# Optimization experiments

Hardware: AMD Instinct MI355X
Metric: run time of the kernel (lower is better)

## Reference

```python
import jax, jax.numpy as jnp
import numpy as np

EPS = 1e-5
NUM_HEADS = 16
HEAD_DIM = 64


def layernorm(x, g, b):
    mu = jnp.mean(x, axis=-1, keepdims=True)
    var = jnp.mean(jnp.square(x - mu), axis=-1, keepdims=True)
    return (x - mu) * jax.lax.rsqrt(var + EPS) * g + b


def setup_inputs() -> dict:
    key = jax.random.key(0)
    ks = jax.random.split(key, 10)
    B, S, Q, D = 4, 4096, 256, 1024
    x = jax.random.normal(ks[0], (B, S, D), dtype=jnp.float32)
    queries = jax.random.normal(ks[1], (B, Q, D), dtype=jnp.float32)
    attn_mask = jax.random.randint(ks[2], (B, NUM_HEADS, Q, S), 0, 2) == 1
    key_padding_mask = jax.random.randint(ks[3], (B, S), 0, 2) == 1
    scale = 1.0 / np.sqrt(2.0 * D)  # xavier-ish
    Wq = jax.random.normal(ks[4], (D, D), dtype=jnp.float32) * scale
    Wk = jax.random.normal(ks[5], (D, D), dtype=jnp.float32) * scale
    Wv = jax.random.normal(ks[6], (D, D), dtype=jnp.float32) * scale
    Wo = jax.random.normal(ks[7], (D, D), dtype=jnp.float32) * scale
    ln1_g = jnp.ones((D,), jnp.float32); ln1_b = jnp.zeros((D,), jnp.float32)
    ln2_g = jnp.ones((D,), jnp.float32); ln2_b = jnp.zeros((D,), jnp.float32)
    return {"x": x, "queries": queries, "attn_mask": attn_mask,
            "key_padding_mask": key_padding_mask, "Wq": Wq, "Wk": Wk,
            "Wv": Wv, "Wo": Wo, "ln1_g": ln1_g, "ln1_b": ln1_b,
            "ln2_g": ln2_g, "ln2_b": ln2_b}


def reference(x, queries, attn_mask, key_padding_mask, Wq, Wk, Wv, Wo,
              ln1_g, ln1_b, ln2_g, ln2_b):
    B, S, D = x.shape
    Q = queries.shape[1]
    H, hd = NUM_HEADS, HEAD_DIM

    xn = layernorm(x, ln1_g, ln1_b)
    q = (queries @ Wq.T).reshape(B, Q, H, hd)
    k = (xn @ Wk.T).reshape(B, S, H, hd)
    v = (xn @ Wv.T).reshape(B, S, H, hd)

    # scores: (B, H, Q, S)
    scores = jnp.einsum('bqhd,bshd->bhqs', q, k) / np.sqrt(hd)

    mask = attn_mask | key_padding_mask[:, None, None, :]
    neg_inf = jnp.float32(-jnp.inf)
    masked = jnp.where(mask, neg_inf, scores)
    all_masked = jnp.all(mask, axis=-1, keepdims=True)  # rows fully masked
    safe = jnp.where(all_masked, 0.0, masked)
    attn = jax.nn.softmax(safe, axis=-1)
    attn = jnp.where(all_masked, 0.0, attn)

    out = jnp.einsum('bhqs,bshd->bqhd', attn, v).reshape(B, Q, D)
    out = layernorm(out, ln2_g, ln2_b)
    return out @ Wo.T, attn.mean(axis=1)
```

## Files before the change

### kernel.cpp

```cpp
#include <hip/hip_runtime.h>
#include <math.h>

#define DEV __device__ __forceinline__

typedef float  f4v  __attribute__((ext_vector_type(4)));
typedef __bf16 b8v  __attribute__((ext_vector_type(8)));
typedef short  s8v  __attribute__((ext_vector_type(8)));

DEV short f2b(float f){ __bf16 h = (__bf16)f; return __builtin_bit_cast(short, h); }
DEV float b2f(short s){ __bf16 h = __builtin_bit_cast(__bf16, s); return (float)h; }

DEV void gload16(const void* g, void* l){
  __builtin_amdgcn_global_load_lds((const __attribute__((address_space(1))) void*)g,
                                   (__attribute__((address_space(3))) void*)l, 16, 0, 0);
}

DEV b8v ldsf(const short* p){ return __builtin_bit_cast(b8v, *(const s8v*)p); }

DEV f4v mfma16(b8v a, b8v b, f4v c){ return __builtin_amdgcn_mfma_f32_16x16x32_bf16(a, b, c, 0, 0, 0); }

DEV void lds_barrier(){
  asm volatile("s_waitcnt lgkmcnt(0)" ::: "memory");
  __builtin_amdgcn_s_barrier();
}

__global__ __launch_bounds__(256) void prep_kernel(const float* __restrict__ x, const float* __restrict__ ln1g,
                                                   const float* __restrict__ ln1b, short* __restrict__ xn,
                                                   const float* __restrict__ s0, const float* __restrict__ s1,
                                                   const float* __restrict__ s2, const float* __restrict__ s3,
                                                   const float* __restrict__ s4,
                                                   short* __restrict__ d0, short* __restrict__ d1,
                                                   short* __restrict__ d2, short* __restrict__ d3,
                                                   short* __restrict__ d4){
  int bid = blockIdx.x, tid = threadIdx.x;
  if (bid < 5120){
    int i = bid*256 + tid;
    int buf = i >> 18, j = i & 262143;
    const float* s = (buf==0)?s0:(buf==1)?s1:(buf==2)?s2:(buf==3)?s3:s4;
    short*       d = (buf==0)?d0:(buf==1)?d1:(buf==2)?d2:(buf==3)?d3:d4;
    float4 v = ((const float4*)s)[j];
    ((short4*)d)[j] = make_short4(f2b(v.x), f2b(v.y), f2b(v.z), f2b(v.w));
    return;
  }
  int row = bid - 5120;
  const float4 v = ((const float4*)(x + (size_t)row*1024))[tid];
  float s = v.x + v.y + v.z + v.w;
  #pragma unroll
  for (int off=1; off<64; off<<=1) s += __shfl_xor(s, off);
  __shared__ float red[4];
  if ((tid&63)==0) red[tid>>6] = s;
  __syncthreads();
  float mu = (red[0]+red[1]+red[2]+red[3]) * (1.0f/1024.0f);
  float e0=v.x-mu, e1=v.y-mu, e2=v.z-mu, e3=v.w-mu;
  float q = e0*e0 + e1*e1 + e2*e2 + e3*e3;
  #pragma unroll
  for (int off=1; off<64; off<<=1) q += __shfl_xor(q, off);
  __syncthreads();
  if ((tid&63)==0) red[tid>>6] = q;
  __syncthreads();
  float rs = rsqrtf((red[0]+red[1]+red[2]+red[3]) * (1.0f/1024.0f) + 1e-5f);
  float4 g4 = ((const float4*)ln1g)[tid];
  float4 b4 = ((const float4*)ln1b)[tid];
  short4 o = make_short4(f2b(e0*rs*g4.x + b4.x), f2b(e1*rs*g4.y + b4.y),
                         f2b(e2*rs*g4.z + b4.z), f2b(e3*rs*g4.w + b4.w));
  ((short4*)(xn + (size_t)row*1024))[tid] = o;
}

__global__ __launch_bounds__(256) void ln_reduce_kernel(const short* __restrict__ opart, const float* __restrict__ gg,
                                                        const float* __restrict__ bb, short* __restrict__ out){
  int row = blockIdx.x, tid = threadIdx.x;
  float a0=0.f, a1=0.f, a2=0.f, a3=0.f;
  #pragma unroll
  for (int sc=0; sc<32; ++sc){
    short4 t = ((const short4*)(opart + ((size_t)sc*1024 + row)*1024))[tid];
    a0 += b2f(t.x); a1 += b2f(t.y); a2 += b2f(t.z); a3 += b2f(t.w);
  }
  float s = a0 + a1 + a2 + a3;
  #pragma unroll
  for (int off=1; off<64; off<<=1) s += __shfl_xor(s, off);
  __shared__ float red[4];
  if ((tid&63)==0) red[tid>>6] = s;
  __syncthreads();
  float mu = (red[0]+red[1]+red[2]+red[3]) * (1.0f/1024.0f);
  float d0=a0-mu, d1=a1-mu, d2=a2-mu, d3=a3-mu;
  float q = d0*d0 + d1*d1 + d2*d2 + d3*d3;
  #pragma unroll
  for (int off=1; off<64; off<<=1) q += __shfl_xor(q, off);
  __syncthreads();
  if ((tid&63)==0) red[tid>>6] = q;
  __syncthreads();
  float rs = rsqrtf((red[0]+red[1]+red[2]+red[3]) * (1.0f/1024.0f) + 1e-5f);
  float4 g4 = ((const float4*)gg)[tid];
  float4 b4 = ((const float4*)bb)[tid];
  short4 o = make_short4(f2b(d0*rs*g4.x + b4.x), f2b(d1*rs*g4.y + b4.y),
                         f2b(d2*rs*g4.z + b4.z), f2b(d3*rs*g4.w + b4.w));
  ((short4*)(out + (size_t)row*1024))[tid] = o;
}

template<int OUTF32>
__global__ __launch_bounds__(256) void gemm_small(const short* __restrict__ A, const short* __restrict__ B,
                                                  void* __restrict__ C, int M, int N, int K){
  __shared__ short sA[2][64*64];
  __shared__ short sB[2][64*64];
  int tid=threadIdx.x, lane=tid&63, wv=tid>>6, g=lane>>4, r=lane&15;
  int wr=wv>>1, wc=wv&1;
  int m0=blockIdx.x*64, n0=blockIdx.y*64;
  f4v z = {0.f,0.f,0.f,0.f};
  f4v acc[2][2];
  #pragma unroll
  for (int i=0;i<2;++i){
    #pragma unroll
    for (int j=0;j<2;++j) acc[i][j]=z;
  }
  auto stage = [&](int buf, int kt){
    #pragma unroll
    for (int i=0;i<2;++i){
      int idx = i*256 + tid;
      int row = idx>>3, cbs = (idx&7)^(row&7);
      gload16(A + (size_t)(m0+row)*K + kt*64 + cbs*8, &sA[buf][(i*256+wv*64)*8]);
      gload16(B + (size_t)(n0+row)*K + kt*64 + cbs*8, &sB[buf][(i*256+wv*64)*8]);
    }
  };
  int nkt = K >> 6;
  stage(0, 0);
  for (int kt=0; kt<nkt; ++kt){
    int cur = kt & 1;
    if (kt+1 < nkt){
      stage(cur^1, kt+1);
      asm volatile("s_waitcnt vmcnt(4)" ::: "memory");
    } else {
      asm volatile("s_waitcnt vmcnt(0)" ::: "memory");
    }
    __builtin_amdgcn_s_barrier();
    b8v af[2][2], bf[2][2];
    #pragma unroll
    for (int mf=0;mf<2;++mf){
      #pragma unroll
      for (int ks=0;ks<2;++ks){
        int ra = wr*32 + mf*16 + r;
        int rb = wc*32 + mf*16 + r;
        af[mf][ks] = ldsf(&sA[cur][ra*64 + (((ks*4+g)^(ra&7))*8)]);
        bf[mf][ks] = ldsf(&sB[cur][rb*64 + (((ks*4+g)^(rb&7))*8)]);
      }
    }
    #pragma unroll
    for (int mf=0;mf<2;++mf){
      #pragma unroll
      for (int nf=0;nf<2;++nf){
        acc[mf][nf] = mfma16(af[mf][0], bf[nf][0], acc[mf][nf]);
        acc[mf][nf] = mfma16(af[mf][1], bf[nf][1], acc[mf][nf]);
      }
    }
    asm volatile("s_waitcnt lgkmcnt(0)" ::: "memory");
    __builtin_amdgcn_s_barrier();
  }
  #pragma unroll
  for (int mf=0;mf<2;++mf){
    #pragma unroll
    for (int nf=0;nf<2;++nf){
      #pragma unroll
      for (int j=0;j<4;++j){
        int m = m0 + wr*32 + mf*16 + g*4 + j;
        int n = n0 + wc*32 + nf*16 + r;
        if (OUTF32) ((float*)C)[(size_t)m*N + n] = acc[mf][nf][j];
        else        ((short*)C)[(size_t)m*N + n] = f2b(acc[mf][nf][j]);
      }
    }
  }
}

__global__ __launch_bounds__(512,2) void gemm_dual_bt(const short* __restrict__ A, const short* __restrict__ B0,
                                                      const short* __restrict__ B1, short* __restrict__ C0,
                                                      short* __restrict__ vt, int M, int N, int K){
  __shared__ short sA[2][256*32];
  __shared__ short sB0[2][128*32];
  __shared__ short sB1[2][128*32];
  int tid=threadIdx.x, lane=tid&63, wv=tid>>6, g=lane>>4, r=lane&15;
  int wr=wv>>1, wc=wv&1;
  int m0=blockIdx.x*256, n0=blockIdx.y*128;
  f4v z = {0.f,0.f,0.f,0.f};
  f4v a0[4][4], a1[4][4];
  #pragma unroll
  for (int i=0;i<4;++i){
    #pragma unroll
    for (int j=0;j<4;++j){ a0[i][j]=z; a1[i][j]=z; }
  }
  auto stage = [&](int buf, int kt){
    #pragma unroll
    for (int i=0;i<2;++i){
      int idx = i*512 + tid;
      int row = idx>>2, sl = (idx&3)^(row&3);
      gload16(A + (size_t)(m0+row)*K + kt*32 + sl*8, &sA[buf][(i*512+wv*64)*8]);
    }
    {
      int row = tid>>2, sl = (tid&3)^(row&3);
      gload16(B0 + (size_t)(n0+row)*K + kt*32 + sl*8, &sB0[buf][(wv*64)*8]);
      gload16(B1 + (size_t)(n0+row)*K + kt*32 + sl*8, &sB1[buf][(wv*64)*8]);
    }
  };
  int nkt = K >> 5;
  stage(0, 0);
  for (int kt=0; kt<nkt; ++kt){
    int cur = kt & 1;
    if (kt+1 < nkt){
      stage(cur^1, kt+1);
      asm volatile("s_waitcnt vmcnt(4)" ::: "memory");
    } else {
      asm volatile("s_waitcnt vmcnt(0)" ::: "memory");
    }
    __builtin_amdgcn_s_barrier();
    b8v af[4], b0f[4], b1f[4];
    #pragma unroll
    for (int mf=0;mf<4;++mf){
      int ra = wr*64+mf*16+r;
      af[mf] = ldsf(&sA[cur][ra*32 + ((g^(ra&3))*8)]);
    }
    #pragma unroll
    for (int nf=0;nf<4;++nf){
      int rb = wc*64+nf*16+r;
      b0f[nf] = ldsf(&sB0[cur][rb*32 + ((g^(rb&3))*8)]);
      b1f[nf] = ldsf(&sB1[cur][rb*32 + ((g^(rb&3))*8)]);
    }
    #pragma unroll
    for (int mf=0;mf<4;++mf){
      #pragma unroll
      for (int nf=0;nf<4;++nf){
        a0[mf][nf] = mfma16(af[mf], b0f[nf], a0[mf][nf]);
        a1[mf][nf] = mfma16(af[mf], b1f[nf], a1[mf][nf]);
      }
    }
    asm volatile("s_waitcnt lgkmcnt(0)" ::: "memory");
    __builtin_amdgcn_s_barrier();
  }
  int b = m0 >> 12;
  #pragma unroll
  for (int mf=0;mf<4;++mf){
    #pragma unroll
    for (int nf=0;nf<4;++nf){
      int m = m0 + wr*64 + mf*16 + g*4;
      int n = n0 + wc*64 + nf*16 + r;
      #pragma unroll
      for (int j=0;j<4;++j)
        C0[(size_t)(m+j)*N + n] = f2b(a0[mf][nf][j]);
      int h = n >> 6, hd = n & 63;
      short4 vv = make_short4(f2b(a1[mf][nf][0]), f2b(a1[mf][nf][1]),
                              f2b(a1[mf][nf][2]), f2b(a1[mf][nf][3]));
      *(short4*)&vt[(size_t)((b*16 + h)*64 + hd)*4096 + (m & 4095)] = vv;
    }
  }
}

__global__ __launch_bounds__(256,2) void lsum_kernel(const short* __restrict__ qp, const short* __restrict__ kb,
                                                     const int* __restrict__ am, const int* __restrict__ kpm,
                                                     unsigned* __restrict__ pm, float* __restrict__ lpart){
  int bid = blockIdx.x;
  int sc = bid & 15, bh = bid >> 4;
  int b = bh >> 4, h = bh & 15;
  int s0 = sc*256;
  __shared__ short sQ[256*64];
  __shared__ short sK[256*64];
  __shared__ unsigned sPM[256*8];
  int tid=threadIdx.x, lane=tid&63, wv=tid>>6, g=lane>>4, r=lane&15;

  #pragma unroll
  for (int i=0;i<8;++i){
    int idx = i*256 + wv*64 + lane;
    int row = idx>>3, cbs = (idx&7)^(row&7);
    gload16(qp + (size_t)(b*256 + row)*1024 + h*64 + cbs*8, &sQ[(i*256+wv*64)*8]);
  }
  #pragma unroll
  for (int i=0;i<8;++i){
    int idx = i*256 + wv*64 + lane;
    int row = idx>>3, cbs = (idx&7)^(row&7);
    gload16(kb + (size_t)(b*4096 + s0 + row)*1024 + h*64 + cbs*8, &sK[(i*256+wv*64)*8]);
  }
  int4 kp = *(const int4*)(kpm + (size_t)b*4096 + s0 + lane*4);
  bool k0 = kp.x!=0, k1 = kp.y!=0, k2 = kp.z!=0, k3 = kp.w!=0;
  #pragma unroll 4
  for (int i=0;i<64;++i){
    int row = wv*64 + i;
    const int4 t = *(const int4*)(am + (size_t)(bh*256 + row)*4096 + s0 + lane*4);
    unsigned long long m0 = __ballot(k0 || (t.x!=0));
    unsigned long long m1 = __ballot(k1 || (t.y!=0));
    unsigned long long m2 = __ballot(k2 || (t.z!=0));
    unsigned long long m3 = __ballot(k3 || (t.w!=0));
    if (lane < 8){
      int jj = lane>>1, hh = lane&1;
      unsigned long long bj = (jj==0)?m0:((jj==1)?m1:((jj==2)?m2:m3));
      unsigned w = (unsigned)(bj >> (hh*32));
      sPM[row*8 + lane] = w;
      pm[(size_t)bid*2048 + row*8 + lane] = w;
    }
  }
  __syncthreads();

  b8v a[4][2];
  #pragma unroll
  for (int mf=0;mf<4;++mf){
    #pragma unroll
    for (int ks=0;ks<2;++ks){
      int q = wv*64 + mf*16 + r;
      a[mf][ks] = ldsf(&sQ[q*64 + (((ks*4+g)^(q&7))*8)]);
    }
  }
  unsigned wmr[4][4][2];
  #pragma unroll
  for (int mf=0;mf<4;++mf){
    #pragma unroll
    for (int jq=0;jq<4;++jq){
      int q = wv*64 + mf*16 + g*4 + jq;
      wmr[mf][jq][0] = sPM[q*8 + (r&3)*2 + 0];
      wmr[mf][jq][1] = sPM[q*8 + (r&3)*2 + 1];
    }
  }
  float lacc[4][4];
  #pragma unroll
  for (int mf=0;mf<4;++mf){
    #pragma unroll
    for (int j=0;j<4;++j) lacc[mf][j] = 0.f;
  }
  f4v z = {0.f,0.f,0.f,0.f};
  #pragma unroll 4
  for (int nf=0;nf<16;++nf){
    int srow = nf*16 + r;
    b8v b0 = ldsf(&sK[srow*64 + ((g^(srow&7))*8)]);
    b8v b1 = ldsf(&sK[srow*64 + (((4+g)^(srow&7))*8)]);
    f4v acc[4];
    #pragma unroll
    for (int mf=0;mf<4;++mf){
      acc[mf] = mfma16(a[mf][0], b0, z);
      acc[mf] = mfma16(a[mf][1], b1, acc[mf]);
    }
    int bitp = 4*(nf&7) + (r>>2);
    #pragma unroll
    for (int mf=0;mf<4;++mf){
      #pragma unroll
      for (int j=0;j<4;++j){
        bool mskd = (wmr[mf][j][nf>>3] >> bitp) & 1u;
        lacc[mf][j] += mskd ? 0.f : __expf(acc[mf][j]*0.125f);
      }
    }
  }
  #pragma unroll
  for (int off=1; off<16; off<<=1){
    #pragma unroll
    for (int mf=0;mf<4;++mf){
      #pragma unroll
      for (int j=0;j<4;++j) lacc[mf][j] += __shfl_xor(lacc[mf][j], off);
    }
  }
  if (r == 0){
    #pragma unroll
    for (int mf=0;mf<4;++mf){
      #pragma unroll
      for (int j=0;j<4;++j){
        int q = wv*64 + mf*16 + g*4 + j;
        lpart[(size_t)bid*256 + q] = lacc[mf][j];
      }
    }
  }
}

__global__ void lcomb_kernel(const float* __restrict__ lpart, float* __restrict__ linv){
  int row = blockIdx.x*256 + threadIdx.x;
  int q = row & 255, bh = row >> 8;
  float l = 0.f;
  #pragma unroll
  for (int sc=0; sc<16; ++sc) l += lpart[(size_t)(bh*16+sc)*256 + q];
  linv[row] = (l > 0.f) ? (1.0f/l) : 0.f;
}

__global__ __launch_bounds__(512,4) void attn_pv_kernel(const short* __restrict__ qp, const short* __restrict__ kb,
                                                        const short* __restrict__ vt, const unsigned* __restrict__ pm,
                                                        const float* __restrict__ linv, short* __restrict__ opart,
                                                        float* __restrict__ out2){
  int bid = blockIdx.x;
  int sc = bid & 31, qt = (bid>>5)&3, b = bid>>7;
  int s0 = sc*128, q0 = qt*64;
  int half = sc & 1, scq = sc >> 1;
  __shared__ short sK[128*64];
  __shared__ short sV[64*128];
  __shared__ short sQ[64*64];
  __shared__ unsigned sPM[64*4];
  int tid=threadIdx.x, lane=tid&63, wv=tid>>6, g=lane>>4, r=lane&15;
  int wq = wv>>2, ws = wv&3;
  f4v z = {0.f,0.f,0.f,0.f};
  float macc[2][2][4];
  #pragma unroll
  for (int sb=0;sb<2;++sb){
    #pragma unroll
    for (int qb=0;qb<2;++qb){
      #pragma unroll
      for (int j=0;j<4;++j) macc[sb][qb][j] = 0.f;
    }
  }

  for (int h=0; h<16; ++h){
    int bh = b*16 + h;
    { int row = tid>>3, cbs = (tid&7)^(row&7);
      gload16(qp + (size_t)(b*256 + q0 + row)*1024 + h*64 + cbs*8, &sQ[(wv*64)*8]); }
    #pragma unroll
    for (int i=0;i<2;++i){
      int idx = i*512 + tid;
      int row = idx>>3, cbs = (idx&7)^(row&7);
      gload16(kb + (size_t)(b*4096 + s0 + row)*1024 + h*64 + cbs*8, &sK[(i*512+wv*64)*8]);
    }
    #pragma unroll
    for (int i=0;i<2;++i){
      int idx = i*512 + tid;
      int row = idx>>4, sl = idx&15, sls = sl^(row&7);
      gload16(vt + (size_t)(bh*64 + row)*4096 + s0 + sls*8, &sV[(i*512+wv*64)*8]);
    }
    if (tid < 256)
      sPM[tid] = pm[(size_t)(bh*16+scq)*2048 + (q0 + (tid>>2))*8 + (tid&3)*2 + half];
    __syncthreads();

    b8v qf[2][2];
    #pragma unroll
    for (int qb=0;qb<2;++qb){
      #pragma unroll
      for (int ks=0;ks<2;++ks){
        int qrow = wq*32 + qb*16 + r;
        qf[qb][ks] = ldsf(&sQ[qrow*64 + (((ks*4+g)^(qrow&7))*8)]);
      }
    }
    f4v accs[2][2];
    __builtin_amdgcn_s_setprio(1);
    #pragma unroll
    for (int sb=0;sb<2;++sb){
      int srow = ws*32 + sb*16 + r;
      b8v k0 = ldsf(&sK[srow*64 + ((g^(srow&7))*8)]);
      b8v k1 = ldsf(&sK[srow*64 + (((4+g)^(srow&7))*8)]);
      #pragma unroll
      for (int qb=0;qb<2;++qb){
        accs[sb][qb] = mfma16(k0, qf[qb][0], z);
        accs[sb][qb] = mfma16(k1, qf[qb][1], accs[sb][qb]);
      }
    }
    __builtin_amdgcn_s_setprio(0);
    lds_barrier();

    float iv[2];
    iv[0] = linv[(size_t)bh*256 + q0 + wq*32 + r];
    iv[1] = linv[(size_t)bh*256 + q0 + wq*32 + 16 + r];
    unsigned wmq[2][4];
    #pragma unroll
    for (int qb=0;qb<2;++qb){
      #pragma unroll
      for (int j=0;j<4;++j)
        wmq[qb][j] = sPM[(wq*32+qb*16+r)*4 + j];
    }
    short* P = &sK[0];
    #pragma unroll
    for (int sb=0;sb<2;++sb){
      int bitp = ws*8 + sb*4 + g;
      #pragma unroll
      for (int qb=0;qb<2;++qb){
        float pj[4];
        #pragma unroll
        for (int j=0;j<4;++j){
          bool mskd = (wmq[qb][j] >> bitp) & 1u;
          pj[j] = mskd ? 0.f : __expf(accs[sb][qb][j]*0.125f) * iv[qb];
          macc[sb][qb][j] += pj[j];
        }
        int q = wq*32 + qb*16 + r;
        unsigned lo = ((unsigned)(unsigned short)f2b(pj[0])) | (((unsigned)(unsigned short)f2b(pj[1]))<<16);
        unsigned hi = ((unsigned)(unsigned short)f2b(pj[2])) | (((unsigned)(unsigned short)f2b(pj[3]))<<16);
        int sbase = (ws*32 + sb*16 + g*4) ^ ((q&7)<<3);
        uint2 pk; pk.x = lo; pk.y = hi;
        *(uint2*)&P[q*128 + sbase] = pk;
      }
    }
    lds_barrier();

    f4v acco[2]; acco[0]=z; acco[1]=z;
    __builtin_amdgcn_s_setprio(1);
    #pragma unroll
    for (int ks=0;ks<4;++ks){
      int vrow = ws*16 + r;
      b8v bv = ldsf(&sV[vrow*128 + ((ks*32+g*8) ^ ((vrow&7)<<3))]);
      #pragma unroll
      for (int mf=0;mf<2;++mf){
        int prow = wq*32 + mf*16 + r;
        b8v ap = ldsf(&P[prow*128 + ((ks*32+g*8) ^ ((prow&7)<<3))]);
        acco[mf] = mfma16(ap, bv, acco[mf]);
      }
    }
    __builtin_amdgcn_s_setprio(0);
    #pragma unroll
    for (int mf=0;mf<2;++mf){
      #pragma unroll
      for (int j=0;j<4;++j)
        opart[((size_t)sc*1024 + b*256 + q0 + wq*32 + mf*16 + g*4 + j)*1024 + h*64 + ws*16 + r] = f2b(acco[mf][j]);
    }
    lds_barrier();
  }

  #pragma unroll
  for (int sb=0;sb<2;++sb){
    #pragma unroll
    for (int qb=0;qb<2;++qb){
      int q = q0 + wq*32 + qb*16 + r;
      float4 o = make_float4(macc[sb][qb][0]*0.0625f, macc[sb][qb][1]*0.0625f,
                             macc[sb][qb][2]*0.0625f, macc[sb][qb][3]*0.0625f);
      *(float4*)&out2[(size_t)(b*256 + q)*4096 + s0 + ws*32 + sb*16 + g*4] = o;
    }
  }
}

extern "C" void kernel_launch(void* const* d_in, const int* in_sizes, int n_in,
                              void* d_out, int out_size, void* d_ws, size_t ws_size,
                              hipStream_t stream){
  const float* x       = (const float*)d_in[0];
  const float* queries = (const float*)d_in[1];
  const int*   am      = (const int*)d_in[2];
  const int*   kpm     = (const int*)d_in[3];
  const float* Wq      = (const float*)d_in[4];
  const float* Wk      = (const float*)d_in[5];
  const float* Wv      = (const float*)d_in[6];
  const float* Wo      = (const float*)d_in[7];
  const float* ln1g    = (const float*)d_in[8];
  const float* ln1b    = (const float*)d_in[9];
  const float* ln2g    = (const float*)d_in[10];
  const float* ln2b    = (const float*)d_in[11];
  float* out0 = (float*)d_out;
  float* out2 = out0 + (size_t)4*256*1024;
  char* ws = (char*)d_ws;

  size_t off = 0;
  auto alloc = [&](size_t bytes){ void* p = ws + off; off += (bytes + 255) & ~(size_t)255; return p; };
  short*    xn   = (short*)alloc(33554432);
  short*    kb   = (short*)alloc(33554432);
  short*    vt   = (short*)alloc(33554432);
  short*    wqb  = (short*)alloc(2097152);
  short*    wkb  = (short*)alloc(2097152);
  short*    wvb  = (short*)alloc(2097152);
  short*    wob  = (short*)alloc(2097152);
  short*    qbf  = (short*)alloc(2097152);
  short*    qpj  = (short*)alloc(2097152);
  unsigned* pmw  = (unsigned*)alloc(8388608);
  float*    lpart= (float*)alloc(1048576);
  float*    linv = (float*)alloc(65536);
  short*    opart= (short*)alloc(67108864);
  short*    onb  = (short*)alloc(2097152);

  prep_kernel<<<21504,256,0,stream>>>(x, ln1g, ln1b, xn,
                                      queries, Wq, Wk, Wv, Wo, qbf, wqb, wkb, wvb, wob);
  gemm_dual_bt<<<dim3(64,8),512,0,stream>>>(xn, wkb, wvb, kb, vt, 16384, 1024, 1024);
  gemm_small<0><<<dim3(16,16),256,0,stream>>>(qbf, wqb, qpj, 1024, 1024, 1024);
  lsum_kernel<<<1024,256,0,stream>>>(qpj, kb, am, kpm, pmw, lpart);
  lcomb_kernel<<<64,256,0,stream>>>(lpart, linv);
  attn_pv_kernel<<<512,512,0,stream>>>(qpj, kb, vt, pmw, linv, opart, out2);
  ln_reduce_kernel<<<1024,256,0,stream>>>(opart, ln2g, ln2b, onb);
  gemm_small<1><<<dim3(16,16),256,0,stream>>>(onb, wob, out0, 1024, 1024, 1024);
}
```

Before: 325.5 us.

## Replace dual K/V GEMM with 256x256-tile 8-wave pipelined GEMM launched twice

New measurement: 323.3 us. About the same (-0.7%).

```diff
diff --git a/kernel.cpp b/kernel.cpp
--- a/kernel.cpp
+++ b/kernel.cpp
@@ -169,83 +169,156 @@
   }
 }
 
-__global__ __launch_bounds__(512,2) void gemm_dual_bt(const short* __restrict__ A, const short* __restrict__ B0,
-                                                      const short* __restrict__ B1, short* __restrict__ C0,
-                                                      short* __restrict__ vt, int M, int N, int K){
-  __shared__ short sA[2][256*32];
-  __shared__ short sB0[2][128*32];
-  __shared__ short sB1[2][128*32];
+template<int VT>
+__global__ __launch_bounds__(512,1) void gemm8_bt(const short* __restrict__ A, const short* __restrict__ B,
+                                                  short* __restrict__ C){
+  __shared__ short sA[2][256*64];
+  __shared__ short sB[2][256*64];
   int tid=threadIdx.x, lane=tid&63, wv=tid>>6, g=lane>>4, r=lane&15;
-  int wr=wv>>1, wc=wv&1;
-  int m0=blockIdx.x*256, n0=blockIdx.y*128;
+  int wr=wv>>2, wc=wv&3;
+  int m0 = blockIdx.x*256, n0 = blockIdx.y*256;
   f4v z = {0.f,0.f,0.f,0.f};
-  f4v a0[4][4], a1[4][4];
-  #pragma unroll
-  for (int i=0;i<4;++i){
-    #pragma unroll
-    for (int j=0;j<4;++j){ a0[i][j]=z; a1[i][j]=z; }
-  }
-  auto stage = [&](int buf, int kt){
-    #pragma unroll
-    for (int i=0;i<2;++i){
-      int idx = i*512 + tid;
-      int row = idx>>2, sl = (idx&3)^(row&3);
-      gload16(A + (size_t)(m0+row)*K + kt*32 + sl*8, &sA[buf][(i*512+wv*64)*8]);
-    }
-    {
-      int row = tid>>2, sl = (tid&3)^(row&3);
-      gload16(B0 + (size_t)(n0+row)*K + kt*32 + sl*8, &sB0[buf][(wv*64)*8]);
-      gload16(B1 + (size_t)(n0+row)*K + kt*32 + sl*8, &sB1[buf][(wv*64)*8]);
+  f4v acc[8][4];
+  #pragma unroll
+  for (int i=0;i<8;++i){
+    #pragma unroll
+    for (int j=0;j<4;++j) acc[i][j]=z;
+  }
+  auto stageA = [&](int buf, int kt, int h){
+    #pragma unroll
+    for (int ii=0; ii<2; ++ii){
+      int idx = ii*512 + tid;
+      int rl = idx>>3, cs = (idx&7)^(rl&7);
+      int rowA = ((rl>>6)<<7) | (h<<6) | (rl&63);
+      gload16(A + (size_t)(m0+rowA)*1024 + kt*64 + cs*8,
+              &sA[buf][(h*1024 + ii*512 + wv*64)*8]);
     }
   };
-  int nkt = K >> 5;
-  stage(0, 0);
-  for (int kt=0; kt<nkt; ++kt){
-    int cur = kt & 1;
-    if (kt+1 < nkt){
-      stage(cur^1, kt+1);
-      asm volatile("s_waitcnt vmcnt(4)" ::: "memory");
-    } else {
-      asm volatile("s_waitcnt vmcnt(0)" ::: "memory");
-    }
+  auto stageB = [&](int buf, int kt, int h){
+    #pragma unroll
+    for (int ii=0; ii<2; ++ii){
+      int idx = ii*512 + tid;
+      int rl = idx>>3, cs = (idx&7)^(rl&7);
+      int rowB = ((rl>>5)<<6) | (h<<5) | (rl&31);
+      gload16(B + (size_t)(n0+rowB)*1024 + kt*64 + cs*8,
+              &sB[buf][(h*1024 + ii*512 + wv*64)*8]);
+    }
+  };
+  stageA(0,0,0); stageB(0,0,0); stageB(0,0,1); stageA(0,0,1);
+
+  b8v af[4][2];
+  b8v bfr[2][2][2];
+  #pragma unroll 2
+  for (int t=0; t<16; ++t){
+    int cur = t&1, nxt = cur^1;
+    asm volatile("s_waitcnt vmcnt(4)" ::: "memory");
     __builtin_amdgcn_s_barrier();
-    b8v af[4], b0f[4], b1f[4];
-    #pragma unroll
-    for (int mf=0;mf<4;++mf){
-      int ra = wr*64+mf*16+r;
-      af[mf] = ldsf(&sA[cur][ra*32 + ((g^(ra&3))*8)]);
-    }
-    #pragma unroll
-    for (int nf=0;nf<4;++nf){
-      int rb = wc*64+nf*16+r;
-      b0f[nf] = ldsf(&sB0[cur][rb*32 + ((g^(rb&3))*8)]);
-      b1f[nf] = ldsf(&sB1[cur][rb*32 + ((g^(rb&3))*8)]);
-    }
-    #pragma unroll
-    for (int mf=0;mf<4;++mf){
-      #pragma unroll
-      for (int nf=0;nf<4;++nf){
-        a0[mf][nf] = mfma16(af[mf], b0f[nf], a0[mf][nf]);
-        a1[mf][nf] = mfma16(af[mf], b1f[nf], a1[mf][nf]);
-      }
-    }
-    asm volatile("s_waitcnt lgkmcnt(0)" ::: "memory");
+    __builtin_amdgcn_sched_barrier(0);
+    if (t < 15) stageA(nxt, t+1, 0);
+    #pragma unroll
+    for (int m=0;m<4;++m){
+      int lr = wr*64 + m*16 + r;
+      #pragma unroll
+      for (int ks=0;ks<2;++ks)
+        af[m][ks] = ldsf(&sA[cur][lr*64 + (((ks*4+g)^(r&7))*8)]);
+    }
+    #pragma unroll
+    for (int n=0;n<2;++n){
+      int lr = wc*32 + n*16 + r;
+      #pragma unroll
+      for (int ks=0;ks<2;++ks)
+        bfr[0][n][ks] = ldsf(&sB[cur][lr*64 + (((ks*4+g)^(r&7))*8)]);
+    }
+    __builtin_amdgcn_s_setprio(1);
+    #pragma unroll
+    for (int m=0;m<4;++m){
+      #pragma unroll
+      for (int n=0;n<2;++n){
+        acc[m][n] = mfma16(af[m][0], bfr[0][n][0], acc[m][n]);
+        acc[m][n] = mfma16(af[m][1], bfr[0][n][1], acc[m][n]);
+      }
+    }
+    __builtin_amdgcn_s_setprio(0);
+    if (t < 15) { asm volatile("s_waitcnt vmcnt(4)" ::: "memory"); }
+    else        { asm volatile("s_waitcnt vmcnt(2)" ::: "memory"); }
     __builtin_amdgcn_s_barrier();
-  }
+    __builtin_amdgcn_sched_barrier(0);
+    if (t < 15) stageB(nxt, t+1, 0);
+    #pragma unroll
+    for (int n=0;n<2;++n){
+      int lr = 128 + wc*32 + n*16 + r;
+      #pragma unroll
+      for (int ks=0;ks<2;++ks)
+        bfr[1][n][ks] = ldsf(&sB[cur][lr*64 + (((ks*4+g)^(r&7))*8)]);
+    }
+    __builtin_amdgcn_s_setprio(1);
+    #pragma unroll
+    for (int m=0;m<4;++m){
+      #pragma unroll
+      for (int n=0;n<2;++n){
+        acc[m][2+n] = mfma16(af[m][0], bfr[1][n][0], acc[m][2+n]);
+        acc[m][2+n] = mfma16(af[m][1], bfr[1][n][1], acc[m][2+n]);
+      }
+    }
+    __builtin_amdgcn_s_setprio(0);
+    if (t < 15) { asm volatile("s_waitcnt vmcnt(4)" ::: "memory"); }
+    else        { asm volatile("s_waitcnt vmcnt(0)" ::: "memory"); }
+    __builtin_amdgcn_s_barrier();
+    __builtin_amdgcn_sched_barrier(0);
+    if (t < 15) stageB(nxt, t+1, 1);
+    #pragma unroll
+    for (int m=0;m<4;++m){
+      int lr = 128 + wr*64 + m*16 + r;
+      #pragma unroll
+      for (int ks=0;ks<2;++ks)
+        af[m][ks] = ldsf(&sA[cur][lr*64 + (((ks*4+g)^(r&7))*8)]);
+    }
+    __builtin_amdgcn_s_setprio(1);
+    #pragma unroll
+    for (int m=0;m<4;++m){
+      #pragma unroll
+      for (int n=0;n<2;++n){
+        acc[4+m][n] = mfma16(af[m][0], bfr[0][n][0], acc[4+m][n]);
+        acc[4+m][n] = mfma16(af[m][1], bfr[0][n][1], acc[4+m][n]);
+      }
+    }
+    __builtin_amdgcn_s_setprio(0);
+    if (t < 15) stageA(nxt, t+1, 1);
+    __builtin_amdgcn_s_setprio(1);
+    #pragma unroll
+    for (int m=0;m<4;++m){
+      #pragma unroll
+      for (int n=0;n<2;++n){
+        acc[4+m][2+n] = mfma16(af[m][0], bfr[1][n][0], acc[4+m][2+n]);
+        acc[4+m][2+n] = mfma16(af[m][1], bfr[1][n][1], acc[4+m][2+n]);
+      }
+    }
+    __builtin_amdgcn_s_setprio(0);
+  }
+
   int b = m0 >> 12;
   #pragma unroll
-  for (int mf=0;mf<4;++mf){
-    #pragma unroll
-    for (int nf=0;nf<4;++nf){
-      int m = m0 + wr*64 + mf*16 + g*4;
-      int n = n0 + wc*64 + nf*16 + r;
-      #pragma unroll
-      for (int j=0;j<4;++j)
-        C0[(size_t)(m+j)*N + n] = f2b(a0[mf][nf][j]);
-      int h = n >> 6, hd = n & 63;
-      short4 vv = make_short4(f2b(a1[mf][nf][0]), f2b(a1[mf][nf][1]),
-                              f2b(a1[mf][nf][2]), f2b(a1[mf][nf][3]));
-      *(short4*)&vt[(size_t)((b*16 + h)*64 + hd)*4096 + (m & 4095)] = vv;
+  for (int mh=0; mh<2; ++mh){
+    #pragma unroll
+    for (int ml=0; ml<4; ++ml){
+      #pragma unroll
+      for (int nh=0; nh<2; ++nh){
+        #pragma unroll
+        for (int nl=0; nl<2; ++nl){
+          f4v a = acc[mh*4+ml][nh*2+nl];
+          int m = m0 + wr*128 + mh*64 + ml*16 + g*4;
+          int n = n0 + wc*64 + nh*32 + nl*16 + r;
+          if (!VT){
+            #pragma unroll
+            for (int j=0;j<4;++j)
+              C[(size_t)(m+j)*1024 + n] = f2b(a[j]);
+          } else {
+            int h = n >> 6, hd = n & 63;
+            short4 vv = make_short4(f2b(a[0]), f2b(a[1]), f2b(a[2]), f2b(a[3]));
+            *(short4*)&C[(size_t)((b*16 + h)*64 + hd)*4096 + (m & 4095)] = vv;
+          }
+        }
+      }
     }
   }
 }
@@ -546,7 +619,8 @@
 
   prep_kernel<<<21504,256,0,stream>>>(x, ln1g, ln1b, xn,
                                       queries, Wq, Wk, Wv, Wo, qbf, wqb, wkb, wvb, wob);
-  gemm_dual_bt<<<dim3(64,8),512,0,stream>>>(xn, wkb, wvb, kb, vt, 16384, 1024, 1024);
+  gemm8_bt<0><<<dim3(64,4),512,0,stream>>>(xn, wkb, kb);
+  gemm8_bt<1><<<dim3(64,4),512,0,stream>>>(xn, wvb, vt);
   gemm_small<0><<<dim3(16,16),256,0,stream>>>(qbf, wqb, qpj, 1024, 1024, 1024);
   lsum_kernel<<<1024,256,0,stream>>>(qpj, kb, am, kpm, pmw, lpart);
   lcomb_kernel<<<64,256,0,stream>>>(lpart, linv);
```
